# Kernel optimization log

Hardware: AMD Instinct MI355X
Metric: run time of the kernel (lower is better)

## Reference

```python
import jax, jax.numpy as jnp
import numpy as np

N = 50000
E = 800000
IN_DIM, HID, OUT_DIM = 768, 256, 128
BN_EPS = 1e-5
NORM_EPS = 1e-12


def setup_inputs() -> dict:
    key = jax.random.key(0)
    ks = jax.random.split(key, 16)
    inp = {
        "x": jax.random.normal(ks[0], (N, IN_DIM), dtype=jnp.float32),
        "edge_index": jax.random.randint(ks[1], (2, E), 0, N, dtype=jnp.int64),
        "edge_weight": jax.random.uniform(ks[2], (E,), dtype=jnp.float32),
        # GCNConv weights (PyG: out = scatter(norm * (x @ W)[src]) + b)
        "W1": jax.random.normal(ks[3], (IN_DIM, HID), dtype=jnp.float32) * 0.02,
        "b1": jnp.zeros((HID,), jnp.float32),
        "W2": jax.random.normal(ks[4], (HID, HID), dtype=jnp.float32) * 0.02,
        "b2": jnp.zeros((HID,), jnp.float32),
        "W3": jax.random.normal(ks[5], (HID, OUT_DIM), dtype=jnp.float32) * 0.02,
        "b3": jnp.zeros((OUT_DIM,), jnp.float32),
        # BatchNorm (eval mode: running stats)
        "bn1_gamma": jnp.ones((HID,), jnp.float32),
        "bn1_beta": jnp.zeros((HID,), jnp.float32),
        "bn1_mean": jax.random.normal(ks[6], (HID,), dtype=jnp.float32) * 0.1,
        "bn1_var": jax.random.uniform(ks[7], (HID,), dtype=jnp.float32) + 0.5,
        "bn2_gamma": jnp.ones((HID,), jnp.float32),
        "bn2_beta": jnp.zeros((HID,), jnp.float32),
        "bn2_mean": jax.random.normal(ks[8], (HID,), dtype=jnp.float32) * 0.1,
        "bn2_var": jax.random.uniform(ks[9], (HID,), dtype=jnp.float32) + 0.5,
    }
    return inp


def _gcn_norm(edge_index, edge_weight, n):
    # add self loops with weight 1 (PyG GCNConv default)
    src = jnp.concatenate([edge_index[0], jnp.arange(n, dtype=edge_index.dtype)])
    dst = jnp.concatenate([edge_index[1], jnp.arange(n, dtype=edge_index.dtype)])
    ew = jnp.concatenate([edge_weight, jnp.ones((n,), edge_weight.dtype)])
    deg = jax.ops.segment_sum(ew, dst, num_segments=n)  # [N]
    dis = jnp.where(deg > 0, jax.lax.rsqrt(deg), 0.0)
    norm = dis[src] * ew * dis[dst]  # [E+N]
    return src, dst, norm


def _gcn_conv(h, W, b, src, dst, norm, n):
    h = h @ W                                  # [N, F_out]
    msg = h[src] * norm[:, None]               # gather + scale, [E+N, F_out]
    out = jax.ops.segment_sum(msg, dst, num_segments=n)  # scatter-add
    return out + b


def _bn_eval(h, gamma, beta, mean, var):
    return (h - mean) * jax.lax.rsqrt(var + BN_EPS) * gamma + beta


def reference(x, edge_index, edge_weight,
              W1, b1, W2, b2, W3, b3,
              bn1_gamma, bn1_beta, bn1_mean, bn1_var,
              bn2_gamma, bn2_beta, bn2_mean, bn2_var):
    n = x.shape[0]
    src, dst, norm = _gcn_norm(edge_index, edge_weight, n)
    h = _gcn_conv(x, W1, b1, src, dst, norm, n)
    h = jax.nn.relu(_bn_eval(h, bn1_gamma, bn1_beta, bn1_mean, bn1_var))
    h = _gcn_conv(h, W2, b2, src, dst, norm, n)
    h = jax.nn.relu(_bn_eval(h, bn2_gamma, bn2_beta, bn2_mean, bn2_var))
    h = _gcn_conv(h, W3, b3, src, dst, norm, n)
    # F.normalize(x, p=2, dim=1): x / max(||x||, eps)
    nrm = jnp.sqrt(jnp.sum(h * h, axis=1, keepdims=True))
    return h / jnp.maximum(nrm, NORM_EPS)
```

## Files before the change

kernel.cpp:

```cpp
#include <hip/hip_runtime.h>
#include <cstddef>

#define NN 50000
#define EE 800000
#define NB 196

typedef __attribute__((ext_vector_type(8))) _Float16 f16x8;
typedef __attribute__((ext_vector_type(4))) _Float16 f16x4;
typedef __attribute__((ext_vector_type(2))) _Float16 f16x2;
typedef __attribute__((ext_vector_type(4))) float f32x4;

__device__ __forceinline__ unsigned pk2h(float a, float b) {
  auto h = __builtin_amdgcn_cvt_pkrtz(a, b);
  return __builtin_bit_cast(unsigned, h);
}

__global__ void k_zero_off(int* __restrict__ off) {
  int i = blockIdx.x * 256 + threadIdx.x;
  if (i <= NN) off[i] = 0;
}

__global__ void k_count(const int* __restrict__ src, const int* __restrict__ dst,
                        int* __restrict__ off) {
  int e = blockIdx.x * 256 + threadIdx.x;
  if (e < EE) {
    int s = src[e], d = dst[e];
    if (s >= 0 && s < NN && d >= 0 && d < NN) atomicAdd(&off[d], 1);
  }
}

__global__ void k_scanA(int* __restrict__ off, int* __restrict__ bsum) {
  __shared__ int sh[256];
  int t = threadIdx.x;
  int idx = blockIdx.x * 256 + t;
  int v = (idx < NN) ? off[idx] : 0;
  sh[t] = v;
  __syncthreads();
  for (int d = 1; d < 256; d <<= 1) {
    int x = (t >= d) ? sh[t - d] : 0;
    __syncthreads();
    sh[t] += x;
    __syncthreads();
  }
  if (idx < NN) off[idx] = sh[t] - v;
  if (t == 255) bsum[blockIdx.x] = sh[255];
}

__global__ void k_scanB(int* __restrict__ bsum, int* __restrict__ bpre,
                        int* __restrict__ off) {
  __shared__ int sh[256];
  int t = threadIdx.x;
  int v = (t < NB) ? bsum[t] : 0;
  sh[t] = v;
  __syncthreads();
  for (int d = 1; d < 256; d <<= 1) {
    int x = (t >= d) ? sh[t - d] : 0;
    __syncthreads();
    sh[t] += x;
    __syncthreads();
  }
  if (t < NB) bpre[t] = sh[t] - v;
  if (t == 255) off[NN] = sh[255];
}

__global__ void k_scanC(int* __restrict__ off, const int* __restrict__ bpre,
                        int* __restrict__ cursor) {
  int idx = blockIdx.x * 256 + threadIdx.x;
  if (idx < NN) {
    int o = off[idx] + bpre[blockIdx.x];
    off[idx] = o;
    cursor[idx] = o;
  }
}

__global__ void k_fill(const int* __restrict__ src, const int* __restrict__ dst,
                       const float* __restrict__ ew, int* __restrict__ cursor,
                       int* __restrict__ csrc, float* __restrict__ cew) {
  int e = blockIdx.x * 256 + threadIdx.x;
  if (e < EE) {
    int s = src[e], d = dst[e];
    if (s >= 0 && s < NN && d >= 0 && d < NN) {
      int p = atomicAdd(&cursor[d], 1);
      csrc[p] = s;
      cew[p] = ew[e];
    }
  }
}

__global__ void k_degdis(const int* __restrict__ off, const float* __restrict__ cew,
                         float* __restrict__ dis) {
  int i = blockIdx.x * 256 + threadIdx.x;
  if (i >= NN) return;
  int e0 = off[i], e1 = off[i + 1];
  float s = 1.0f;
  for (int e = e0; e < e1; ++e) s += cew[e];
  dis[i] = rsqrtf(s);
}

__global__ void k_affine(const float* __restrict__ g1, const float* __restrict__ be1,
                         const float* __restrict__ m1, const float* __restrict__ v1,
                         const float* __restrict__ g2, const float* __restrict__ be2,
                         const float* __restrict__ m2, const float* __restrict__ v2,
                         float* __restrict__ s1, float* __restrict__ u1,
                         float* __restrict__ s2, float* __restrict__ u2) {
  int f = threadIdx.x;
  float a1 = g1[f] * rsqrtf(v1[f] + 1e-5f);
  s1[f] = a1; u1[f] = be1[f] - m1[f] * a1;
  float a2 = g2[f] * rsqrtf(v2[f] + 1e-5f);
  s2[f] = a2; u2[f] = be2[f] - m2[f] * a2;
}

__global__ void k_wt(const float* __restrict__ W, _Float16* __restrict__ WT,
                     int K, int N) {
  int k = blockIdx.x * 256 + threadIdx.x;
  int n = blockIdx.y;
  if (k < K) WT[(size_t)n * K + k] = (_Float16)W[(size_t)k * N + n];
}

#define LDA 40
template <int A32>
__global__ __launch_bounds__(256) void k_gemm(const void* __restrict__ Ain,
                                              const _Float16* __restrict__ BT,
                                              _Float16* __restrict__ C,
                                              int M, int K, int Nout) {
  __shared__ _Float16 As[2][64 * LDA];
  __shared__ _Float16 Bs[2][128 * LDA];
  const int tid = threadIdx.x;
  const int bm = blockIdx.y << 6;
  const int bn = blockIdx.x << 7;
  const int lane = tid & 63;
  const int wid = tid >> 6;
  const int wm = (wid & 1) << 5;
  const int wn = (wid >> 1) << 6;
  const int quad = lane >> 4;
  const int l16 = lane & 15;

  const int srow = tid >> 2, skc = tid & 3;
  const int agr = bm + srow;
  const int aok = (agr < M);
  const _Float16* ap16 = (const _Float16*)Ain + (size_t)agr * K + (skc << 3);
  const float* ap32 = (const float*)Ain + (size_t)agr * K + (skc << 3);
  const _Float16* bp0 = BT + (size_t)(bn + srow) * K + (skc << 3);
  const _Float16* bp1 = BT + (size_t)(bn + 64 + srow) * K + (skc << 3);

  f32x4 acc[2][4] = {};

  uint4 a16_0, a16_1;
  float4 a32lo_0, a32hi_0, a32lo_1, a32hi_1;
  uint4 b0_0, b1_0, b0_1, b1_1;

#define ISSUE(S, k0)                                                        \
  do {                                                                      \
    if (A32) {                                                              \
      if (aok) {                                                            \
        a32lo_##S = *(const float4*)(ap32 + (k0));                          \
        a32hi_##S = *(const float4*)(ap32 + (k0) + 4);                      \
      } else {                                                              \
        a32lo_##S = make_float4(0.f, 0.f, 0.f, 0.f);                       \
        a32hi_##S = make_float4(0.f, 0.f, 0.f, 0.f);                       \
      }                                                                     \
    } else {                                                                \
      a16_##S = aok ? *(const uint4*)(ap16 + (k0)) : make_uint4(0, 0, 0, 0);\
    }                                                                       \
    b0_##S = *(const uint4*)(bp0 + (k0));                                   \
    b1_##S = *(const uint4*)(bp1 + (k0));                                   \
  } while (0)

#define COMMIT(S, buf)                                                      \
  do {                                                                      \
    uint4 va;                                                               \
    if (A32) {                                                              \
      va.x = pk2h(a32lo_##S.x, a32lo_##S.y);                                \
      va.y = pk2h(a32lo_##S.z, a32lo_##S.w);                                \
      va.z = pk2h(a32hi_##S.x, a32hi_##S.y);                                \
      va.w = pk2h(a32hi_##S.z, a32hi_##S.w);                                \
    } else {                                                                \
      va = a16_##S;                                                         \
    }                                                                       \
    *(uint4*)&As[buf][srow * LDA + (skc << 3)] = va;                        \
    *(uint4*)&Bs[buf][srow * LDA + (skc << 3)] = b0_##S;                    \
    *(uint4*)&Bs[buf][(64 + srow) * LDA + (skc << 3)] = b1_##S;             \
  } while (0)

#define COMPUTE(buf)                                                        \
  do {                                                                      \
    f16x8 af[2], bfr[4];                                                    \
    _Pragma("unroll") for (int mt = 0; mt < 2; ++mt)                        \
        af[mt] = *(const f16x8*)&As[buf][(wm + (mt << 4) + l16) * LDA + (quad << 3)]; \
    _Pragma("unroll") for (int nt = 0; nt < 4; ++nt)                        \
        bfr[nt] = *(const f16x8*)&Bs[buf][(wn + (nt << 4) + l16) * LDA + (quad << 3)]; \
    _Pragma("unroll") for (int mt = 0; mt < 2; ++mt)                        \
        _Pragma("unroll") for (int nt = 0; nt < 4; ++nt)                    \
            acc[mt][nt] = __builtin_amdgcn_mfma_f32_16x16x32_f16(af[mt], bfr[nt], acc[mt][nt], 0, 0, 0); \
  } while (0)

  const int T = K >> 5;

  ISSUE(0, 0);
  COMMIT(0, 0);
  if (T > 1) ISSUE(1, 32);
  __syncthreads();

  for (int t = 0; t < T; t += 2) {
    if (t + 2 < T) ISSUE(0, (t + 2) << 5);
    COMPUTE(0);
    if (t + 1 < T) COMMIT(1, 1);
    __syncthreads();
    if (t + 1 < T) {
      if (t + 3 < T) ISSUE(1, (t + 3) << 5);
      COMPUTE(1);
      if (t + 2 < T) COMMIT(0, 0);
      __syncthreads();
    }
  }
#undef ISSUE
#undef COMMIT
#undef COMPUTE

  const int rbase = bm + wm + (quad << 2);
#pragma unroll
  for (int mt = 0; mt < 2; ++mt) {
#pragma unroll
    for (int reg = 0; reg < 4; ++reg) {
      int r = rbase + (mt << 4) + reg;
      if (r < M) {
        _Float16* crow = C + (size_t)r * Nout + bn + wn + l16;
#pragma unroll
        for (int nt = 0; nt < 4; ++nt) crow[nt << 4] = (_Float16)acc[mt][nt][reg];
      }
    }
  }
}

__global__ __launch_bounds__(256) void k_agg256(const _Float16* __restrict__ hW,
                                                const float* __restrict__ dis,
                                                const float* __restrict__ b,
                                                const int* __restrict__ off,
                                                const int* __restrict__ csrc,
                                                const float* __restrict__ cew,
                                                const float* __restrict__ s,
                                                const float* __restrict__ u,
                                                _Float16* __restrict__ hout) {
  int i = (blockIdx.x << 2) + (threadIdx.x >> 6);
  if (i >= NN) return;
  int lane = threadIdx.x & 63;
  float di = dis[i];
  float4 bb = *(const float4*)(b + (lane << 2));
  f16x4 hv = *(const f16x4*)(hW + (size_t)i * 256 + (lane << 2));
  float d2 = di * di;
  float4 acc;
  acc.x = fmaf((float)hv.x, d2, bb.x);
  acc.y = fmaf((float)hv.y, d2, bb.y);
  acc.z = fmaf((float)hv.z, d2, bb.z);
  acc.w = fmaf((float)hv.w, d2, bb.w);
  int e0 = off[i], e1 = off[i + 1];
  int e = e0;
  for (; e + 3 < e1; e += 4) {
    int sa = csrc[e], sb = csrc[e + 1], sc = csrc[e + 2], sd = csrc[e + 3];
    float wa = dis[sa] * cew[e] * di;
    float wb = dis[sb] * cew[e + 1] * di;
    float wc = dis[sc] * cew[e + 2] * di;
    float wd = dis[sd] * cew[e + 3] * di;
    f16x4 ra = *(const f16x4*)(hW + (size_t)sa * 256 + (lane << 2));
    f16x4 rb = *(const f16x4*)(hW + (size_t)sb * 256 + (lane << 2));
    f16x4 rc = *(const f16x4*)(hW + (size_t)sc * 256 + (lane << 2));
    f16x4 rd = *(const f16x4*)(hW + (size_t)sd * 256 + (lane << 2));
    acc.x = fmaf((float)ra.x, wa, acc.x); acc.y = fmaf((float)ra.y, wa, acc.y);
    acc.z = fmaf((float)ra.z, wa, acc.z); acc.w = fmaf((float)ra.w, wa, acc.w);
    acc.x = fmaf((float)rb.x, wb, acc.x); acc.y = fmaf((float)rb.y, wb, acc.y);
    acc.z = fmaf((float)rb.z, wb, acc.z); acc.w = fmaf((float)rb.w, wb, acc.w);
    acc.x = fmaf((float)rc.x, wc, acc.x); acc.y = fmaf((float)rc.y, wc, acc.y);
    acc.z = fmaf((float)rc.z, wc, acc.z); acc.w = fmaf((float)rc.w, wc, acc.w);
    acc.x = fmaf((float)rd.x, wd, acc.x); acc.y = fmaf((float)rd.y, wd, acc.y);
    acc.z = fmaf((float)rd.z, wd, acc.z); acc.w = fmaf((float)rd.w, wd, acc.w);
  }
  for (; e < e1; ++e) {
    int sa = csrc[e];
    float wa = dis[sa] * cew[e] * di;
    f16x4 ra = *(const f16x4*)(hW + (size_t)sa * 256 + (lane << 2));
    acc.x = fmaf((float)ra.x, wa, acc.x); acc.y = fmaf((float)ra.y, wa, acc.y);
    acc.z = fmaf((float)ra.z, wa, acc.z); acc.w = fmaf((float)ra.w, wa, acc.w);
  }
  float4 sv = *(const float4*)(s + (lane << 2));
  float4 uv = *(const float4*)(u + (lane << 2));
  float r0 = fmaxf(fmaf(acc.x, sv.x, uv.x), 0.f);
  float r1 = fmaxf(fmaf(acc.y, sv.y, uv.y), 0.f);
  float r2 = fmaxf(fmaf(acc.z, sv.z, uv.z), 0.f);
  float r3 = fmaxf(fmaf(acc.w, sv.w, uv.w), 0.f);
  uint2 pk;
  pk.x = pk2h(r0, r1);
  pk.y = pk2h(r2, r3);
  *(uint2*)&hout[(size_t)i * 256 + (lane << 2)] = pk;
}

__global__ __launch_bounds__(256) void k_agg128_l2(const _Float16* __restrict__ hW,
                                                   const float* __restrict__ dis,
                                                   const float* __restrict__ b,
                                                   const int* __restrict__ off,
                                                   const int* __restrict__ csrc,
                                                   const float* __restrict__ cew,
                                                   float* __restrict__ out) {
  int i = (blockIdx.x << 2) + (threadIdx.x >> 6);
  if (i >= NN) return;
  int lane = threadIdx.x & 63;
  float di = dis[i];
  float2 bb = *(const float2*)(b + (lane << 1));
  f16x2 hv = *(const f16x2*)(hW + (size_t)i * 128 + (lane << 1));
  float d2 = di * di;
  float2 acc;
  acc.x = fmaf((float)hv.x, d2, bb.x);
  acc.y = fmaf((float)hv.y, d2, bb.y);
  int e0 = off[i], e1 = off[i + 1];
  int e = e0;
  for (; e + 3 < e1; e += 4) {
    int sa = csrc[e], sb = csrc[e + 1], sc = csrc[e + 2], sd = csrc[e + 3];
    float wa = dis[sa] * cew[e] * di;
    float wb = dis[sb] * cew[e + 1] * di;
    float wc = dis[sc] * cew[e + 2] * di;
    float wd = dis[sd] * cew[e + 3] * di;
    f16x2 ra = *(const f16x2*)(hW + (size_t)sa * 128 + (lane << 1));
    f16x2 rb = *(const f16x2*)(hW + (size_t)sb * 128 + (lane << 1));
    f16x2 rc = *(const f16x2*)(hW + (size_t)sc * 128 + (lane << 1));
    f16x2 rd = *(const f16x2*)(hW + (size_t)sd * 128 + (lane << 1));
    acc.x = fmaf((float)ra.x, wa, acc.x); acc.y = fmaf((float)ra.y, wa, acc.y);
    acc.x = fmaf((float)rb.x, wb, acc.x); acc.y = fmaf((float)rb.y, wb, acc.y);
    acc.x = fmaf((float)rc.x, wc, acc.x); acc.y = fmaf((float)rc.y, wc, acc.y);
    acc.x = fmaf((float)rd.x, wd, acc.x); acc.y = fmaf((float)rd.y, wd, acc.y);
  }
  for (; e < e1; ++e) {
    int sa = csrc[e];
    float wa = dis[sa] * cew[e] * di;
    f16x2 ra = *(const f16x2*)(hW + (size_t)sa * 128 + (lane << 1));
    acc.x = fmaf((float)ra.x, wa, acc.x); acc.y = fmaf((float)ra.y, wa, acc.y);
  }
  float ss = fmaf(acc.x, acc.x, acc.y * acc.y);
#pragma unroll
  for (int o = 32; o > 0; o >>= 1) ss += __shfl_xor(ss, o, 64);
  float sc2 = 1.0f / fmaxf(sqrtf(ss), 1e-12f);
  acc.x *= sc2;
  acc.y *= sc2;
  *(float2*)(out + (size_t)i * 128 + (lane << 1)) = acc;
}

extern "C" void kernel_launch(void* const* d_in, const int* in_sizes, int n_in,
                              void* d_out, int out_size, void* d_ws, size_t ws_size,
                              hipStream_t stream) {
  const size_t OFF_CUR = 50176, OFF_BS = 100352, OFF_BP = 100608;
  const size_t OFF_CS = 100864, OFF_CW = 900864, OFF_DIS = 1700864;
  const size_t OFF_AFF = 1751040, OFF_HW = 1752064;
  const size_t OFF_HB = OFF_HW + (size_t)NN * 256;
  const size_t OFF_WT1 = OFF_HB + (size_t)NN * 128;
  const size_t OFF_WT2 = OFF_WT1 + 768 * 256 / 2;
  const size_t OFF_WT3 = OFF_WT2 + 256 * 256 / 2;
  const size_t WS_UNITS = OFF_WT3 + 256 * 128 / 2 + 256;
  if (ws_size < WS_UNITS * 4) return;

  const float* x  = (const float*)d_in[0];
  const int* ei   = (const int*)d_in[1];
  const float* ew = (const float*)d_in[2];
  const float* W1 = (const float*)d_in[3];
  const float* b1 = (const float*)d_in[4];
  const float* W2 = (const float*)d_in[5];
  const float* b2 = (const float*)d_in[6];
  const float* W3 = (const float*)d_in[7];
  const float* b3 = (const float*)d_in[8];
  const float* g1 = (const float*)d_in[9];
  const float* be1 = (const float*)d_in[10];
  const float* m1 = (const float*)d_in[11];
  const float* v1 = (const float*)d_in[12];
  const float* g2 = (const float*)d_in[13];
  const float* be2 = (const float*)d_in[14];
  const float* m2 = (const float*)d_in[15];
  const float* v2 = (const float*)d_in[16];
  float* out = (float*)d_out;
  const int* src = ei;
  const int* dstp = ei + EE;

  int* wsi = (int*)d_ws;
  float* wsf = (float*)d_ws;
  int* off = wsi;
  int* cursor = wsi + OFF_CUR;
  int* bsum = wsi + OFF_BS;
  int* bpre = wsi + OFF_BP;
  int* csrc = wsi + OFF_CS;
  float* cew = wsf + OFF_CW;
  float* dis = wsf + OFF_DIS;
  float* s1 = wsf + OFF_AFF;
  float* u1 = s1 + 256;
  float* s2 = u1 + 256;
  float* u2 = s2 + 256;
  _Float16* hW = (_Float16*)(wsf + OFF_HW);
  _Float16* hb = (_Float16*)(wsi + OFF_HB);
  _Float16* wT1 = (_Float16*)(wsi + OFF_WT1);
  _Float16* wT2 = (_Float16*)(wsi + OFF_WT2);
  _Float16* wT3 = (_Float16*)(wsi + OFF_WT3);

  dim3 b256(256);
  const int EB = (EE + 255) / 256;
  k_zero_off<<<NB, b256, 0, stream>>>(off);
  k_count<<<EB, b256, 0, stream>>>(src, dstp, off);
  k_scanA<<<NB, b256, 0, stream>>>(off, bsum);
  k_scanB<<<1, b256, 0, stream>>>(bsum, bpre, off);
  k_scanC<<<NB, b256, 0, stream>>>(off, bpre, cursor);
  k_fill<<<EB, b256, 0, stream>>>(src, dstp, ew, cursor, csrc, cew);
  k_degdis<<<NB, b256, 0, stream>>>(off, cew, dis);
  k_affine<<<1, b256, 0, stream>>>(g1, be1, m1, v1, g2, be2, m2, v2, s1, u1, s2, u2);
  k_wt<<<dim3(3, 256), b256, 0, stream>>>(W1, wT1, 768, 256);
  k_wt<<<dim3(1, 256), b256, 0, stream>>>(W2, wT2, 256, 256);
  k_wt<<<dim3(1, 128), b256, 0, stream>>>(W3, wT3, 256, 128);

  const int GM = (NN + 63) / 64;
  const int AGB = (NN + 3) / 4;
  k_gemm<1><<<dim3(2, GM), b256, 0, stream>>>(x, wT1, hW, NN, 768, 256);
  k_agg256<<<AGB, b256, 0, stream>>>(hW, dis, b1, off, csrc, cew, s1, u1, hb);
  k_gemm<0><<<dim3(2, GM), b256, 0, stream>>>(hb, wT2, hW, NN, 256, 256);
  k_agg256<<<AGB, b256, 0, stream>>>(hW, dis, b2, off, csrc, cew, s2, u2, hb);
  k_gemm<0><<<dim3(1, GM), b256, 0, stream>>>(hb, wT3, hW, NN, 256, 128);
  k_agg128_l2<<<AGB, b256, 0, stream>>>(hW, dis, b3, off, csrc, cew, out);
}
```

Before: 608.8 us.

## Widen GEMM K-tile to 64 with single-buffered LDS and register prefetch

Result: faster. 582.3 us (-4.4%).

```diff
diff --git a/kernel.cpp b/kernel.cpp
--- a/kernel.cpp
+++ b/kernel.cpp
@@ -117,14 +117,14 @@
   if (k < K) WT[(size_t)n * K + k] = (_Float16)W[(size_t)k * N + n];
 }
 
-#define LDA 40
+#define LDA 72
 template <int A32>
 __global__ __launch_bounds__(256) void k_gemm(const void* __restrict__ Ain,
                                               const _Float16* __restrict__ BT,
                                               _Float16* __restrict__ C,
                                               int M, int K, int Nout) {
-  __shared__ _Float16 As[2][64 * LDA];
-  __shared__ _Float16 Bs[2][128 * LDA];
+  __shared__ _Float16 As[64 * LDA];
+  __shared__ _Float16 Bs[128 * LDA];
   const int tid = threadIdx.x;
   const int bm = blockIdx.y << 6;
   const int bn = blockIdx.x << 7;
@@ -135,81 +135,95 @@
   const int quad = lane >> 4;
   const int l16 = lane & 15;
 
-  const int srow = tid >> 2, skc = tid & 3;
-  const int agr = bm + srow;
-  const int aok = (agr < M);
-  const _Float16* ap16 = (const _Float16*)Ain + (size_t)agr * K + (skc << 3);
-  const float* ap32 = (const float*)Ain + (size_t)agr * K + (skc << 3);
+  const int srow = tid >> 3, skc = tid & 7;
+  const int agr0 = bm + srow, agr1 = bm + srow + 32;
+  const int aok0 = (agr0 < M), aok1 = (agr1 < M);
+  const float* ap32_0 = (const float*)Ain + (size_t)agr0 * K + (skc << 3);
+  const float* ap32_1 = (const float*)Ain + (size_t)agr1 * K + (skc << 3);
+  const _Float16* ap16_0 = (const _Float16*)Ain + (size_t)agr0 * K + (skc << 3);
+  const _Float16* ap16_1 = (const _Float16*)Ain + (size_t)agr1 * K + (skc << 3);
   const _Float16* bp0 = BT + (size_t)(bn + srow) * K + (skc << 3);
-  const _Float16* bp1 = BT + (size_t)(bn + 64 + srow) * K + (skc << 3);
+  const _Float16* bp1 = BT + (size_t)(bn + 32 + srow) * K + (skc << 3);
+  const _Float16* bp2 = BT + (size_t)(bn + 64 + srow) * K + (skc << 3);
+  const _Float16* bp3 = BT + (size_t)(bn + 96 + srow) * K + (skc << 3);
 
   f32x4 acc[2][4] = {};
 
-  uint4 a16_0, a16_1;
-  float4 a32lo_0, a32hi_0, a32lo_1, a32hi_1;
-  uint4 b0_0, b1_0, b0_1, b1_1;
-
-#define ISSUE(S, k0)                                                        \
-  do {                                                                      \
-    if (A32) {                                                              \
-      if (aok) {                                                            \
-        a32lo_##S = *(const float4*)(ap32 + (k0));                          \
-        a32hi_##S = *(const float4*)(ap32 + (k0) + 4);                      \
-      } else {                                                              \
-        a32lo_##S = make_float4(0.f, 0.f, 0.f, 0.f);                       \
-        a32hi_##S = make_float4(0.f, 0.f, 0.f, 0.f);                       \
-      }                                                                     \
-    } else {                                                                \
-      a16_##S = aok ? *(const uint4*)(ap16 + (k0)) : make_uint4(0, 0, 0, 0);\
-    }                                                                       \
-    b0_##S = *(const uint4*)(bp0 + (k0));                                   \
-    b1_##S = *(const uint4*)(bp1 + (k0));                                   \
+  uint4 ra0, ra1;
+  float4 ra0lo, ra0hi, ra1lo, ra1hi;
+  uint4 rb0, rb1, rb2, rb3;
+
+#define ISSUE(k0)                                                             \
+  do {                                                                        \
+    if (A32) {                                                                \
+      if (aok0) {                                                             \
+        ra0lo = *(const float4*)(ap32_0 + (k0));                              \
+        ra0hi = *(const float4*)(ap32_0 + (k0) + 4);                          \
+      } else {                                                                \
+        ra0lo = make_float4(0.f, 0.f, 0.f, 0.f);                              \
+        ra0hi = make_float4(0.f, 0.f, 0.f, 0.f);                              \
+      }                                                                       \
+      if (aok1) {                                                             \
+        ra1lo = *(const float4*)(ap32_1 + (k0));                              \
+        ra1hi = *(const float4*)(ap32_1 + (k0) + 4);                          \
+      } else {                                                                \
+        ra1lo = make_float4(0.f, 0.f, 0.f, 0.f);                              \
+        ra1hi = make_float4(0.f, 0.f, 0.f, 0.f);                              \
+      }                                                                       \
+    } else {                                                                  \
+      ra0 = aok0 ? *(const uint4*)(ap16_0 + (k0)) : make_uint4(0, 0, 0, 0);   \
+      ra1 = aok1 ? *(const uint4*)(ap16_1 + (k0)) : make_uint4(0, 0, 0, 0);   \
+    }                                                                         \
+    rb0 = *(const uint4*)(bp0 + (k0));                                        \
+    rb1 = *(const uint4*)(bp1 + (k0));                                        \
+    rb2 = *(const uint4*)(bp2 + (k0));                                        \
+    rb3 = *(const uint4*)(bp3 + (k0));                                        \
   } while (0)
 
-#define COMMIT(S, buf)                                                      \
-  do {                                                                      \
-    uint4 va;                                                               \
-    if (A32) {                                                              \
-      va.x = pk2h(a32lo_##S.x, a32lo_##S.y);                                \
-      va.y = pk2h(a32lo_##S.z, a32lo_##S.w);                                \
-      va.z = pk2h(a32hi_##S.x, a32hi_##S.y);                                \
-      va.w = pk2h(a32hi_##S.z, a32hi_##S.w);                                \
-    } else {                                                                \
-      va = a16_##S;                                                         \
-    }                                                                       \
-    *(uint4*)&As[buf][srow * LDA + (skc << 3)] = va;                        \
-    *(uint4*)&Bs[buf][srow * LDA + (skc << 3)] = b0_##S;                    \
-    *(uint4*)&Bs[buf][(64 + srow) * LDA + (skc << 3)] = b1_##S;             \
+#define COMMIT()                                                              \
+  do {                                                                        \
+    uint4 va0, va1;                                                           \
+    if (A32) {                                                                \
+      va0.x = pk2h(ra0lo.x, ra0lo.y); va0.y = pk2h(ra0lo.z, ra0lo.w);         \
+      va0.z = pk2h(ra0hi.x, ra0hi.y); va0.w = pk2h(ra0hi.z, ra0hi.w);         \
+      va1.x = pk2h(ra1lo.x, ra1lo.y); va1.y = pk2h(ra1lo.z, ra1lo.w);         \
+      va1.z = pk2h(ra1hi.x, ra1hi.y); va1.w = pk2h(ra1hi.z, ra1hi.w);         \
+    } else {                                                                  \
+      va0 = ra0; va1 = ra1;                                                   \
+    }                                                                         \
+    *(uint4*)&As[srow * LDA + (skc << 3)] = va0;                              \
+    *(uint4*)&As[(srow + 32) * LDA + (skc << 3)] = va1;                       \
+    *(uint4*)&Bs[srow * LDA + (skc << 3)] = rb0;                              \
+    *(uint4*)&Bs[(srow + 32) * LDA + (skc << 3)] = rb1;                       \
+    *(uint4*)&Bs[(srow + 64) * LDA + (skc << 3)] = rb2;                       \
+    *(uint4*)&Bs[(srow + 96) * LDA + (skc << 3)] = rb3;                       \
   } while (0)
 
-#define COMPUTE(buf)                                                        \
-  do {                                                                      \
-    f16x8 af[2], bfr[4];                                                    \
-    _Pragma("unroll") for (int mt = 0; mt < 2; ++mt)                        \
-        af[mt] = *(const f16x8*)&As[buf][(wm + (mt << 4) + l16) * LDA + (quad << 3)]; \
-    _Pragma("unroll") for (int nt = 0; nt < 4; ++nt)                        \
-        bfr[nt] = *(const f16x8*)&Bs[buf][(wn + (nt << 4) + l16) * LDA + (quad << 3)]; \
-    _Pragma("unroll") for (int mt = 0; mt < 2; ++mt)                        \
-        _Pragma("unroll") for (int nt = 0; nt < 4; ++nt)                    \
-            acc[mt][nt] = __builtin_amdgcn_mfma_f32_16x16x32_f16(af[mt], bfr[nt], acc[mt][nt], 0, 0, 0); \
+#define COMPUTE()                                                             \
+  do {                                                                        \
+    _Pragma("unroll") for (int s = 0; s < 2; ++s) {                           \
+      f16x8 af[2], bfr[4];                                                    \
+      _Pragma("unroll") for (int mt = 0; mt < 2; ++mt)                        \
+          af[mt] = *(const f16x8*)&As[(wm + (mt << 4) + l16) * LDA + (s << 5) + (quad << 3)]; \
+      _Pragma("unroll") for (int nt = 0; nt < 4; ++nt)                        \
+          bfr[nt] = *(const f16x8*)&Bs[(wn + (nt << 4) + l16) * LDA + (s << 5) + (quad << 3)]; \
+      _Pragma("unroll") for (int mt = 0; mt < 2; ++mt)                        \
+          _Pragma("unroll") for (int nt = 0; nt < 4; ++nt)                    \
+              acc[mt][nt] = __builtin_amdgcn_mfma_f32_16x16x32_f16(af[mt], bfr[nt], acc[mt][nt], 0, 0, 0); \
+    }                                                                         \
   } while (0)
 
-  const int T = K >> 5;
-
-  ISSUE(0, 0);
-  COMMIT(0, 0);
-  if (T > 1) ISSUE(1, 32);
+  const int T = K >> 6;
+
+  ISSUE(0);
+  COMMIT();
   __syncthreads();
-
-  for (int t = 0; t < T; t += 2) {
-    if (t + 2 < T) ISSUE(0, (t + 2) << 5);
-    COMPUTE(0);
-    if (t + 1 < T) COMMIT(1, 1);
+  for (int t = 0; t < T; ++t) {
+    if (t + 1 < T) ISSUE((t + 1) << 6);
+    COMPUTE();
     __syncthreads();
     if (t + 1 < T) {
-      if (t + 3 < T) ISSUE(1, (t + 3) << 5);
-      COMPUTE(1);
-      if (t + 2 < T) COMMIT(0, 0);
+      COMMIT();
       __syncthreads();
     }
   }
```
